# Kernel tuning notes

Hardware: AMD Instinct MI355X
Metric: run time of the kernel (lower is better)

Reference implementation:

```python
import jax, jax.numpy as jnp
import numpy as np

B, T, C, L = 128, 1024, 128, 128
EPS = 1e-7        # keras.backend.epsilon()
NEG = -1e30       # log-space -inf surrogate


def setup_inputs() -> dict:
    key = jax.random.key(0)
    k1, k2, k3, k4 = jax.random.split(key, 4)
    logits = jax.random.normal(k1, (B, T, C), dtype=jnp.float32)
    y_pred = jax.nn.softmax(logits, axis=-1)                      # ctc_batch_cost expects probs
    y_true = jax.random.randint(k2, (B, L), 0, C - 1)             # blank = C-1 excluded from labels
    input_len = jax.random.randint(k3, (B, 1), T // 2, T + 1)
    label_len = jax.random.randint(k4, (B, 1), L // 2, L + 1)
    return {"y_true": y_true, "y_pred": y_pred, "input_len": input_len, "label_len": label_len}


def _ctc_loss(y_pred, y_true, input_len, label_len):
    # Faithful port of keras ctc_batch_cost: blank index = C-1, merge repeated,
    # log(y_pred + eps), returns per-sample loss with shape [B, 1].
    log_probs = jnp.log(y_pred + EPS)                             # [B,T,C]
    b, t_max, c = log_probs.shape
    blank = c - 1
    l = y_true.shape[1]
    s = 2 * l + 1
    # extended label sequence: blank, l1, blank, l2, ..., blank   [B,S]
    ext = jnp.full((b, s), blank, dtype=y_true.dtype).at[:, 1::2].set(y_true)
    # emission log-prob of each extended symbol at each frame     [B,T,S]
    lp_ext = jnp.take_along_axis(
        log_probs, jnp.broadcast_to(ext[:, None, :], (b, t_max, s)), axis=2)
    # skip transition s-2 -> s allowed iff ext[s] != blank and ext[s] != ext[s-2]
    allow_skip = jnp.concatenate(
        [jnp.zeros((b, 2), bool), (ext[:, 2:] != blank) & (ext[:, 2:] != ext[:, :-2])], axis=1)
    alpha0 = jnp.full((b, s), NEG, dtype=log_probs.dtype).at[:, 0].set(0.0)
    in_len = input_len.reshape(b, 1).astype(jnp.int32)

    def step(alpha, xt):
        lp_t, t = xt                                              # lp_t: [B,S]
        a1 = jnp.pad(alpha[:, :-1], ((0, 0), (1, 0)), constant_values=NEG)
        a2 = jnp.where(allow_skip,
                       jnp.pad(alpha[:, :-2], ((0, 0), (2, 0)), constant_values=NEG), NEG)
        new = lp_t + jnp.logaddexp(jnp.logaddexp(alpha, a1), a2)
        new = jnp.where(t < in_len, new, alpha)                   # freeze past input_len
        return new, None

    alpha, _ = jax.lax.scan(step, alpha0, (jnp.swapaxes(lp_ext, 0, 1), jnp.arange(t_max)))
    lab = label_len.reshape(b, 1).astype(jnp.int32)
    a_last = jnp.take_along_axis(alpha, 2 * lab, axis=1)          # ends at final blank
    a_prev = jnp.take_along_axis(alpha, jnp.maximum(2 * lab - 1, 0), axis=1)  # or final label
    return -jnp.logaddexp(a_last, a_prev)                         # [B,1]


def reference(y_true, y_pred, input_len, label_len):
    return _ctc_loss(y_pred, y_true, input_len, label_len)
```

## Files before the change

kernel.cpp:

```cpp
#include <hip/hip_runtime.h>
#include <cstdint>

#define NB 128
#define NT 1024
#define NC 128
#define NL 128
#define NS 257
#define EPSF 1e-7f
#define LN2F 0.69314718055994530942f
#define NEGL2 -1.442695e30f

typedef float __attribute__((ext_vector_type(2))) v2f;

__device__ __forceinline__ float fexp2(float x){ return __builtin_amdgcn_exp2f(x); }
__device__ __forceinline__ float flog2(float x){ return __builtin_amdgcn_logf(x); }

__device__ __forceinline__ float shup1(float x){
    int r = __builtin_amdgcn_update_dpp(0, __float_as_int(x), 0x138, 0xf, 0xf, true);
    return __int_as_float(r);
}
__device__ __forceinline__ int shup1i(int x){
    return __builtin_amdgcn_update_dpp(0, x, 0x138, 0xf, 0xf, true);
}

__device__ __forceinline__ void dma16(const float* g, float* lds){
    __builtin_amdgcn_global_load_lds((const __attribute__((address_space(1))) void*)g,
                                     (__attribute__((address_space(3))) void*)lds,
                                     16, 0, 0);
}

#define VM_DRAIN() asm volatile("s_waitcnt vmcnt(0)" ::: "memory")

#define AS3U(p) ((unsigned)(size_t)(__attribute__((address_space(3))) void*)(p))

#define WAITLGKM(N) do{ asm volatile("s_waitcnt lgkmcnt(" #N ")" ::: "memory"); \
                        __builtin_amdgcn_sched_barrier(0); }while(0)

#define FILLA(S, O0,O1,O2,O3) do{ \
  asm volatile("ds_read2st64_b32 %0, %1 offset0:" #O0 " offset1:" #O1 : "=v"(S##B2[0]) : "v"(aB)); \
  asm volatile("ds_read2st64_b32 %0, %1 offset0:" #O2 " offset1:" #O3 : "=v"(S##B2[1]) : "v"(aB)); \
  asm volatile("ds_read2st64_b32 %0, %1 offset0:" #O0 " offset1:" #O1 : "=v"(S##A2[0]) : "v"(aA)); \
  asm volatile("ds_read2st64_b32 %0, %1 offset0:" #O2 " offset1:" #O3 : "=v"(S##A2[1]) : "v"(aA)); \
  asm volatile("ds_read2st64_b32 %0, %1 offset0:" #O0 " offset1:" #O1 : "=v"(S##C2[0]) : "v"(aC)); \
  asm volatile("ds_read2st64_b32 %0, %1 offset0:" #O2 " offset1:" #O3 : "=v"(S##C2[1]) : "v"(aC)); \
}while(0)

#define GROUP(S, gg) do{ \
    const v2f pb0 = S##B2[0] + E2, pa0 = S##A2[0] + E2, pc0 = S##C2[0] + E2; \
    const v2f pb1 = S##B2[1] + E2, pa1 = S##A2[1] + E2, pc1 = S##C2[1] + E2; \
    { const bool c_ = !freeze || ((k*32 + (gg)*4 + 0) < Tn); step1(pb0.x, pa0.x, pc0.x, c_); } \
    shm3 = shup1(m3); \
    { const bool c_ = !freeze || ((k*32 + (gg)*4 + 1) < Tn); step1(pb0.y, pa0.y, pc0.y, c_); } \
    shm3 = shup1(m3); \
    { const bool c_ = !freeze || ((k*32 + (gg)*4 + 2) < Tn); step1(pb1.x, pa1.x, pc1.x, c_); } \
    shm3 = shup1(m3); \
    { const bool c_ = !freeze || ((k*32 + (gg)*4 + 3) < Tn); step1(pb1.y, pa1.y, pc1.y, c_); } \
    boundary(early); }while(0)

__global__ __launch_bounds__(64,1)
void ctc_fwd_kernel(const int* __restrict__ y_true,
                    const float* __restrict__ y_pred,
                    const int* __restrict__ input_len,
                    const int* __restrict__ label_len,
                    float* __restrict__ out)
{
    __shared__ float buf[2][32 * NC];
    __shared__ float lg_alpha[NS + 3];

    const int b    = blockIdx.x;
    const int lane = threadIdx.x;
    const float* __restrict__ base = y_pred + (size_t)b * NT * NC;

    int Tn = input_len[b];
    Tn = Tn < 0 ? 0 : (Tn > NT ? NT : Tn);

    const int* __restrict__ yrow = y_true + b * NL;
    const int y0v = yrow[2 * lane]     & (NC - 1);
    const int y1v = yrow[2 * lane + 1] & (NC - 1);
    const int yp  = shup1i(y1v);
    const bool skip1 = (lane > 0) && (y0v != yp);
    const bool skip3 = (y1v != y0v);
    const bool isl0  = (lane == 0);
    const bool isl63 = (lane == 63);
    const float skip3f = skip3 ? 1.f : 0.f;

    const v2f E2 = { EPSF, EPSF };

    float m0 = isl0 ? 1.f : 0.f, m1 = 0.f, m2 = 0.f, m3 = 0.f, m4 = 0.f;
    int   ei  = 0;
    float f0  = 1.f;
    float fs1 = skip1 ? 1.f : 0.f;
    float shm3 = 0.f;

    v2f s0B2[2], s0A2[2], s0C2[2];
    v2f s1B2[2], s1A2[2], s1C2[2];
    v2f s2B2[2], s2A2[2], s2C2[2];

    auto dma_chunk = [&](int c){
        const float* gsrc = base + (size_t)c * 32 * NC;
        float* dst = &buf[c & 1][0];
        #pragma unroll
        for (int i = 0; i < 16; ++i)
            dma16(gsrc + i * 256 + lane * 4, dst + i * 256);
    };

    auto step1 = [&](float Pb, float Pa, float Pc, bool commit){
        float a1  = m3 + m2;
        float a2  = m2 + m1;
        float s43 = m4 + m3;
        float a5  = m1 + m0;
        float a6  = fmaf(m1,   skip3f, a1);
        float a7  = fmaf(shm3, fs1,    a5);
        float a4  = fmaf(shm3, f0,     m0);
        float n3 = Pc * a6;
        float n2 = Pb * a2;
        float n4 = Pb * s43;
        float n0 = Pb * a4;
        float n1 = Pa * a7;
        if (commit) { m0 = n0; m1 = n1; m2 = n2; m3 = n3; m4 = n4; }
    };

    auto boundary = [&](bool early){
        float mx = fmaxf(fmaxf(m0, m1), fmaxf(m2, m3));
        if (isl63) mx = fmaxf(mx, m4);
        const uint32_t bx = __float_as_uint(mx);
        const int eb = (int)(bx >> 23);
        const float inv = __uint_as_float((uint32_t)(254 - eb) << 23);
        const int de = eb - 127;
        int s_nb;
        if (early) {
            const bool dead = (mx == 0.f);
            int e1 = dead ? ei : (ei + de);
            int s1 = shup1i(e1);
            int e2 = (dead && !isl0) ? s1 : e1;
            int s2 = shup1i(e2);
            ei = (dead && !isl0) ? s2 : e2;
            s_nb = s2;
        } else {
            ei += de;
            s_nb = shup1i(ei);
        }
        int d = s_nb - ei;
        d = d < -126 ? -126 : (d > 126 ? 126 : d);
        f0 = __uint_as_float((uint32_t)(d + 127) << 23);
        fs1 = skip1 ? f0 : 0.f;
        m0 *= inv; m1 *= inv; m2 *= inv; m3 *= inv; m4 *= inv;
        shm3 = shup1(m3);
    };

    auto chunkbody = [&](int k, bool early, bool freeze){
        const int h = k & 1;
        const unsigned aB = AS3U(&buf[h][NC - 1]);
        const unsigned aA = AS3U(&buf[h][y0v]);
        const unsigned aC = AS3U(&buf[h][y1v]);

        FILLA(s0,  0, 2, 4, 6);
        if (k + 1 < 32) dma_chunk(k + 1);
        FILLA(s1,  8,10,12,14);

        FILLA(s2, 16,18,20,22); WAITLGKM(12); GROUP(s0, 0);
        FILLA(s0, 24,26,28,30); WAITLGKM(12); GROUP(s1, 1);
        FILLA(s1, 32,34,36,38); WAITLGKM(12); GROUP(s2, 2);
        FILLA(s2, 40,42,44,46); WAITLGKM(12); GROUP(s0, 3);
        FILLA(s0, 48,50,52,54); WAITLGKM(12); GROUP(s1, 4);
        FILLA(s1, 56,58,60,62); WAITLGKM(12); GROUP(s2, 5);
                                WAITLGKM(6);  GROUP(s0, 6);
                                WAITLGKM(0);  GROUP(s1, 7);

        VM_DRAIN();
    };

    dma_chunk(0);
    VM_DRAIN();

    const int nfull = Tn >> 5;
    #pragma unroll 1
    for (int k = 0; k < 8; ++k)       chunkbody(k, true,  false);
    #pragma unroll 1
    for (int k = 8; k < nfull; ++k)   chunkbody(k, false, false);
    if (nfull < 32 && (Tn & 31))      chunkbody(nfull, false, true);

    const float e = (float)ei;
    lg_alpha[4 * lane + 0] = (m0 > 0.f) ? (e + flog2(m0)) : NEGL2;
    lg_alpha[4 * lane + 1] = (m1 > 0.f) ? (e + flog2(m1)) : NEGL2;
    lg_alpha[4 * lane + 2] = (m2 > 0.f) ? (e + flog2(m2)) : NEGL2;
    lg_alpha[4 * lane + 3] = (m3 > 0.f) ? (e + flog2(m3)) : NEGL2;
    if (isl63) lg_alpha[256] = (m4 > 0.f) ? (e + flog2(m4)) : NEGL2;
    __syncthreads();

    if (lane == 0) {
        int lab = label_len[b];
        lab = lab < 0 ? 0 : (lab > NL ? NL : lab);
        const int i_last = 2 * lab;
        const int i_prev = i_last > 0 ? i_last - 1 : 0;
        float A  = lg_alpha[i_last];
        float Bv = lg_alpha[i_prev];
        float mx = fmaxf(A, Bv);
        float r;
        if (mx < -1.0e29f) {
            r = mx;
        } else {
            float s = fexp2(A - mx) + fexp2(Bv - mx);
            r = mx + flog2(s);
        }
        out[b] = -r * LN2F;
    }
}

extern "C" void kernel_launch(void* const* d_in, const int* in_sizes, int n_in,
                              void* d_out, int out_size, void* d_ws, size_t ws_size,
                              hipStream_t stream) {
    const int*   y_true    = (const int*)d_in[0];
    const float* y_pred    = (const float*)d_in[1];
    const int*   input_len = (const int*)d_in[2];
    const int*   label_len = (const int*)d_in[3];
    float* outp = (float*)d_out;
    ctc_fwd_kernel<<<dim3(NB), dim3(64), 0, stream>>>(y_true, y_pred, input_len, label_len, outp);
}
```

Baseline: 134.5 us.

## Pack eight batch rows per block and halve the frame chunk size

Each block now runs eight wavefronts, one per batch row, instead of one, so the grid shrinks from 128 single-wave blocks to 16 blocks of 512 threads. Each wave's double-buffered LDS staging now holds 16 frames instead of 32, so the eight buffers fit in shared memory. The loop bounds, DMA count and software-pipelined read groups are rescaled to match. The final log-alpha scratch reuses the wave's own buffer and replaces the block barrier with a local lgkm wait. This may lower launch and per-block overhead, but the whole serial recurrence now runs on only 16 CUs with several waves per SIMD, and per-chunk drain overhead doubles.

```diff
diff --git a/kernel.cpp b/kernel.cpp
--- a/kernel.cpp
+++ b/kernel.cpp
@@ -2,7 +2,10 @@
 #include <cstdint>
 
 #define NB 128
+#define NBW 8
 #define NT 1024
+#define NR 16
+#define NCHUNK (NT / NR)
 #define NC 128
 #define NL 128
 #define NS 257
@@ -48,27 +51,28 @@
 #define GROUP(S, gg) do{ \
     const v2f pb0 = S##B2[0] + E2, pa0 = S##A2[0] + E2, pc0 = S##C2[0] + E2; \
     const v2f pb1 = S##B2[1] + E2, pa1 = S##A2[1] + E2, pc1 = S##C2[1] + E2; \
-    { const bool c_ = !freeze || ((k*32 + (gg)*4 + 0) < Tn); step1(pb0.x, pa0.x, pc0.x, c_); } \
+    { const bool c_ = !freeze || ((k*NR + (gg)*4 + 0) < Tn); step1(pb0.x, pa0.x, pc0.x, c_); } \
     shm3 = shup1(m3); \
-    { const bool c_ = !freeze || ((k*32 + (gg)*4 + 1) < Tn); step1(pb0.y, pa0.y, pc0.y, c_); } \
+    { const bool c_ = !freeze || ((k*NR + (gg)*4 + 1) < Tn); step1(pb0.y, pa0.y, pc0.y, c_); } \
     shm3 = shup1(m3); \
-    { const bool c_ = !freeze || ((k*32 + (gg)*4 + 2) < Tn); step1(pb1.x, pa1.x, pc1.x, c_); } \
+    { const bool c_ = !freeze || ((k*NR + (gg)*4 + 2) < Tn); step1(pb1.x, pa1.x, pc1.x, c_); } \
     shm3 = shup1(m3); \
-    { const bool c_ = !freeze || ((k*32 + (gg)*4 + 3) < Tn); step1(pb1.y, pa1.y, pc1.y, c_); } \
+    { const bool c_ = !freeze || ((k*NR + (gg)*4 + 3) < Tn); step1(pb1.y, pa1.y, pc1.y, c_); } \
     boundary(early); }while(0)
 
-__global__ __launch_bounds__(64,1)
+__global__ __launch_bounds__(64 * NBW, 1)
 void ctc_fwd_kernel(const int* __restrict__ y_true,
                     const float* __restrict__ y_pred,
                     const int* __restrict__ input_len,
                     const int* __restrict__ label_len,
                     float* __restrict__ out)
 {
-    __shared__ float buf[2][32 * NC];
-    __shared__ float lg_alpha[NS + 3];
-
-    const int b    = blockIdx.x;
-    const int lane = threadIdx.x;
+    __shared__ __align__(16) float buf[NBW][2][NR * NC];
+
+    const int tid  = threadIdx.x;
+    const int w    = tid >> 6;
+    const int lane = tid & 63;
+    const int b    = blockIdx.x * NBW + w;
     const float* __restrict__ base = y_pred + (size_t)b * NT * NC;
 
     int Tn = input_len[b];
@@ -97,10 +101,10 @@
     v2f s2B2[2], s2A2[2], s2C2[2];
 
     auto dma_chunk = [&](int c){
-        const float* gsrc = base + (size_t)c * 32 * NC;
-        float* dst = &buf[c & 1][0];
+        const float* gsrc = base + (size_t)c * NR * NC;
+        float* dst = &buf[w][c & 1][0];
         #pragma unroll
-        for (int i = 0; i < 16; ++i)
+        for (int i = 0; i < 8; ++i)
             dma16(gsrc + i * 256 + lane * 4, dst + i * 256);
     };
 
@@ -150,22 +154,18 @@
 
     auto chunkbody = [&](int k, bool early, bool freeze){
         const int h = k & 1;
-        const unsigned aB = AS3U(&buf[h][NC - 1]);
-        const unsigned aA = AS3U(&buf[h][y0v]);
-        const unsigned aC = AS3U(&buf[h][y1v]);
+        const unsigned aB = AS3U(&buf[w][h][NC - 1]);
+        const unsigned aA = AS3U(&buf[w][h][y0v]);
+        const unsigned aC = AS3U(&buf[w][h][y1v]);
 
         FILLA(s0,  0, 2, 4, 6);
-        if (k + 1 < 32) dma_chunk(k + 1);
+        if (k + 1 < NCHUNK) dma_chunk(k + 1);
         FILLA(s1,  8,10,12,14);
 
         FILLA(s2, 16,18,20,22); WAITLGKM(12); GROUP(s0, 0);
         FILLA(s0, 24,26,28,30); WAITLGKM(12); GROUP(s1, 1);
-        FILLA(s1, 32,34,36,38); WAITLGKM(12); GROUP(s2, 2);
-        FILLA(s2, 40,42,44,46); WAITLGKM(12); GROUP(s0, 3);
-        FILLA(s0, 48,50,52,54); WAITLGKM(12); GROUP(s1, 4);
-        FILLA(s1, 56,58,60,62); WAITLGKM(12); GROUP(s2, 5);
-                                WAITLGKM(6);  GROUP(s0, 6);
-                                WAITLGKM(0);  GROUP(s1, 7);
+                                WAITLGKM(6);  GROUP(s2, 2);
+                                WAITLGKM(0);  GROUP(s0, 3);
 
         VM_DRAIN();
     };
@@ -173,28 +173,29 @@
     dma_chunk(0);
     VM_DRAIN();
 
-    const int nfull = Tn >> 5;
+    const int nfull = Tn >> 4;
     #pragma unroll 1
-    for (int k = 0; k < 8; ++k)       chunkbody(k, true,  false);
+    for (int k = 0; k < 16; ++k)      chunkbody(k, true,  false);
     #pragma unroll 1
-    for (int k = 8; k < nfull; ++k)   chunkbody(k, false, false);
-    if (nfull < 32 && (Tn & 31))      chunkbody(nfull, false, true);
-
+    for (int k = 16; k < nfull; ++k)  chunkbody(k, false, false);
+    if (nfull < NCHUNK && (Tn & 15))  chunkbody(nfull, false, true);
+
+    float* lg = &buf[w][0][0];
     const float e = (float)ei;
-    lg_alpha[4 * lane + 0] = (m0 > 0.f) ? (e + flog2(m0)) : NEGL2;
-    lg_alpha[4 * lane + 1] = (m1 > 0.f) ? (e + flog2(m1)) : NEGL2;
-    lg_alpha[4 * lane + 2] = (m2 > 0.f) ? (e + flog2(m2)) : NEGL2;
-    lg_alpha[4 * lane + 3] = (m3 > 0.f) ? (e + flog2(m3)) : NEGL2;
-    if (isl63) lg_alpha[256] = (m4 > 0.f) ? (e + flog2(m4)) : NEGL2;
-    __syncthreads();
+    lg[4 * lane + 0] = (m0 > 0.f) ? (e + flog2(m0)) : NEGL2;
+    lg[4 * lane + 1] = (m1 > 0.f) ? (e + flog2(m1)) : NEGL2;
+    lg[4 * lane + 2] = (m2 > 0.f) ? (e + flog2(m2)) : NEGL2;
+    lg[4 * lane + 3] = (m3 > 0.f) ? (e + flog2(m3)) : NEGL2;
+    if (isl63) lg[256] = (m4 > 0.f) ? (e + flog2(m4)) : NEGL2;
+    asm volatile("s_waitcnt lgkmcnt(0)" ::: "memory");
 
     if (lane == 0) {
         int lab = label_len[b];
         lab = lab < 0 ? 0 : (lab > NL ? NL : lab);
         const int i_last = 2 * lab;
         const int i_prev = i_last > 0 ? i_last - 1 : 0;
-        float A  = lg_alpha[i_last];
-        float Bv = lg_alpha[i_prev];
+        float A  = lg[i_last];
+        float Bv = lg[i_prev];
         float mx = fmaxf(A, Bv);
         float r;
         if (mx < -1.0e29f) {
@@ -215,5 +216,5 @@
     const int*   input_len = (const int*)d_in[2];
     const int*   label_len = (const int*)d_in[3];
     float* outp = (float*)d_out;
-    ctc_fwd_kernel<<<dim3(NB), dim3(64), 0, stream>>>(y_true, y_pred, input_len, label_len, outp);
-}
+    ctc_fwd_kernel<<<dim3(NB / NBW), dim3(64 * NBW), 0, stream>>>(y_true, y_pred, input_len, label_len, outp);
+}
```

Measured after the change: 167.7 us. +24.7%, slower.
